# Performance work log

Hardware: AMD Instinct MI355X
Metric: run time of the kernel (lower is better)

Reference implementation:

```python
import jax, jax.numpy as jnp
import numpy as np
import math

HIDDEN = 2048
NUM_HEADS = 16
HEAD_SIZE = HIDDEN // NUM_HEADS
BATCH = 2
SEQ = 2048


def setup_inputs() -> dict:
    key = jax.random.key(0)
    k_x, k_wq, k_bq, k_wo, k_bo = jax.random.split(key, 5)
    scale_in = 1.0 / math.sqrt(HIDDEN)
    return {
        "x": jax.random.normal(k_x, (BATCH, SEQ, HIDDEN), dtype=jnp.float32),
        # torch Linear stored as W[out,in]; we keep the jax-friendly transpose [in,out]
        "Wqkv": jax.random.normal(k_wq, (HIDDEN, 3 * HIDDEN), dtype=jnp.float32) * scale_in,
        "bqkv": jax.random.normal(k_bq, (3 * HIDDEN,), dtype=jnp.float32) * 0.01,
        "Wo": jax.random.normal(k_wo, (HIDDEN, HIDDEN), dtype=jnp.float32) * scale_in,
        "bo": jax.random.normal(k_bo, (HIDDEN,), dtype=jnp.float32) * 0.01,
    }


def reference(x, Wqkv, bqkv, Wo, bo):
    b, s, _ = x.shape
    # fused QKV projection; channel layout is (three, num_heads, head_size)
    kqv = x @ Wqkv + bqkv                      # [b, s, 3*hidden]
    kqv = kqv.reshape(b, s, 3, NUM_HEADS, HEAD_SIZE)
    q = kqv[:, :, 0]                           # [b, s, n, h]
    k = kqv[:, :, 1]
    v = kqv[:, :, 2]
    # scores[b, n, s_key, t_query] = K_s . Q_t, scaled
    scores = jnp.einsum('bsnh,btnh->bnst', k, q) / math.sqrt(HEAD_SIZE)
    # faithful to original: keep upper triangle (key <= query), masked entries are exactly -10000
    ones = jnp.ones_like(scores)
    scores = jnp.triu(scores) + (-10000.0) * jnp.tril(ones, k=-1)
    attn = jax.nn.softmax(scores, axis=2)      # softmax over key dim
    out = jnp.einsum('bnkq,bknh->bqnh', attn, v)  # [b, s, n, h]
    out = out.reshape(b, s, NUM_HEADS * HEAD_SIZE)
    return out @ Wo + bo
```

## Files before the change

kernel.cpp:

```cpp
#include <hip/hip_runtime.h>
#include <hip/hip_bf16.h>

typedef __hip_bfloat16 bf16;
typedef __attribute__((ext_vector_type(8))) short short8;
typedef __attribute__((ext_vector_type(8))) unsigned short ushort8;
typedef __attribute__((ext_vector_type(4))) float floatx4;

#define BATCH 2
#define S_LEN 2048
#define NHEAD 16
#define HD 128
#define HIDDEN 2048
#define QSCALE 0.12754435f

static __device__ __forceinline__ unsigned short f2bf(float f) {
    union { float f; unsigned int u; } c; c.f = f;
    unsigned int u = c.u;
    unsigned int rounded = u + 0x7FFF + ((u >> 16) & 1);
    return (unsigned short)(rounded >> 16);
}

__global__ __launch_bounds__(256) void cast_f32_bf16(const float* __restrict__ src,
                                                     bf16* __restrict__ dst) {
    int i = (blockIdx.x * 256 + threadIdx.x) * 8;
    float4 a = *(const float4*)&src[i];
    float4 b = *(const float4*)&src[i + 4];
    ushort8 o;
    o[0] = f2bf(a.x); o[1] = f2bf(a.y); o[2] = f2bf(a.z); o[3] = f2bf(a.w);
    o[4] = f2bf(b.x); o[5] = f2bf(b.y); o[6] = f2bf(b.z); o[7] = f2bf(b.w);
    *(ushort8*)&dst[i] = o;
}

__global__ __launch_bounds__(256) void cast_transpose(const float* __restrict__ src,
                                                      bf16* __restrict__ dst,
                                                      int R, int C) {
    __shared__ unsigned short t[32][33];
    int tx = threadIdx.x & 31, ty = threadIdx.x >> 5;
    int c0 = blockIdx.x * 32, r0 = blockIdx.y * 32;
#pragma unroll
    for (int i = 0; i < 4; i++) {
        int r = r0 + ty + i * 8;
        t[ty + i * 8][tx] = f2bf(src[(size_t)r * C + c0 + tx]);
    }
    __syncthreads();
#pragma unroll
    for (int i = 0; i < 4; i++) {
        int cc = c0 + ty + i * 8;
        ((unsigned short*)dst)[(size_t)cc * R + r0 + tx] = t[tx][ty + i * 8];
    }
}

__global__ __launch_bounds__(256) void gemm_bt(const bf16* __restrict__ A,
                                               const bf16* __restrict__ Bt,
                                               const float* __restrict__ bias,
                                               float* __restrict__ C,
                                               bf16* __restrict__ Qb,
                                               bf16* __restrict__ Kb,
                                               bf16* __restrict__ Vt,
                                               int M, int N, int K, int mode) {
    __shared__ __align__(16) bf16 As[128 * 32];
    __shared__ __align__(16) bf16 Bs[128 * 32];

    int tid = threadIdx.x;
    int wave = tid >> 6, lane = tid & 63;
    int quad = lane >> 4, lr = lane & 15;
    int wm = wave >> 1, wn = wave & 1;
    int m0 = blockIdx.y * 128, n0 = blockIdx.x * 128;

    const floatx4 fzero = {0.f, 0.f, 0.f, 0.f};
    floatx4 acc[4][4];
#pragma unroll
    for (int i = 0; i < 4; i++)
#pragma unroll
        for (int j = 0; j < 4; j++) acc[i][j] = fzero;

    int rsub = lane >> 2;
    int csub = (lane & 3) * 8;
    const bf16* gA0 = A + (size_t)(m0 + wave * 32 + rsub) * K + csub;
    const bf16* gA1 = gA0 + (size_t)16 * K;
    const bf16* gB0 = Bt + (size_t)(n0 + wave * 32 + rsub) * K + csub;
    const bf16* gB1 = gB0 + (size_t)16 * K;
    bf16* lA0 = As + wave * 1024;
    bf16* lA1 = As + wave * 1024 + 512;
    bf16* lB0 = Bs + wave * 1024;
    bf16* lB1 = Bs + wave * 1024 + 512;

    for (int kt = 0; kt < K; kt += 32) {
        __builtin_amdgcn_global_load_lds(
            (const __attribute__((address_space(1))) void*)(gA0 + kt),
            (__attribute__((address_space(3))) void*)lA0, 16, 0, 0);
        __builtin_amdgcn_global_load_lds(
            (const __attribute__((address_space(1))) void*)(gA1 + kt),
            (__attribute__((address_space(3))) void*)lA1, 16, 0, 0);
        __builtin_amdgcn_global_load_lds(
            (const __attribute__((address_space(1))) void*)(gB0 + kt),
            (__attribute__((address_space(3))) void*)lB0, 16, 0, 0);
        __builtin_amdgcn_global_load_lds(
            (const __attribute__((address_space(1))) void*)(gB1 + kt),
            (__attribute__((address_space(3))) void*)lB1, 16, 0, 0);
        __syncthreads();

        short8 aF[4], bF[4];
#pragma unroll
        for (int i = 0; i < 4; i++)
            aF[i] = *(const short8*)(As + (wm * 64 + i * 16 + lr) * 32 + quad * 8);
#pragma unroll
        for (int j = 0; j < 4; j++)
            bF[j] = *(const short8*)(Bs + (wn * 64 + j * 16 + lr) * 32 + quad * 8);
#pragma unroll
        for (int i = 0; i < 4; i++)
#pragma unroll
            for (int j = 0; j < 4; j++)
                acc[i][j] = __builtin_amdgcn_mfma_f32_16x16x32_bf16(aF[i], bF[j], acc[i][j], 0, 0, 0);
        __syncthreads();
    }

#pragma unroll
    for (int i = 0; i < 4; i++) {
#pragma unroll
        for (int j = 0; j < 4; j++) {
            int gcn = n0 + wn * 64 + j * 16 + lr;
            float bv = bias[gcn];
#pragma unroll
            for (int reg = 0; reg < 4; reg++) {
                int gm = m0 + wm * 64 + i * 16 + quad * 4 + reg;
                float v = acc[i][j][reg] + bv;
                if (mode == 0) {
                    int t = gcn >> 11, hh = (gcn >> 7) & 15, d = gcn & 127;
                    int bb = gm >> 11, s = gm & 2047;
                    size_t hb = (size_t)(bb * NHEAD + hh);
                    if (t == 0) {
                        Qb[(hb * S_LEN + s) * HD + d] = __float2bfloat16(v * QSCALE);
                    } else if (t == 1) {
                        Kb[(hb * S_LEN + s) * HD + d] = __float2bfloat16(v);
                    } else {
                        Vt[(hb * HD + d) * S_LEN + s] = __float2bfloat16(v);
                    }
                } else {
                    C[(size_t)gm * N + gcn] = v;
                }
            }
        }
    }
}

__global__ __launch_bounds__(256, 1) void attn_kernel(const bf16* __restrict__ Qb,
                                                      const bf16* __restrict__ Kb,
                                                      const bf16* __restrict__ Vt,
                                                      bf16* __restrict__ Obuf) {
    __shared__ __align__(16) bf16 Ks[128][136];
    __shared__ __align__(16) bf16 Vs[128][136];
    __shared__ __align__(16) bf16 Ps[4][32][144];

    int tid = threadIdx.x;
    int wave = tid >> 6, lane = tid & 63;
    int quad = lane >> 4, lr = lane & 15;
    int p = blockIdx.x, head = blockIdx.y, b = blockIdx.z;
    size_t hb = (size_t)(b * NHEAD + head);
    const bf16* Qbase = Qb + hb * S_LEN * HD;
    const bf16* Kbase = Kb + hb * S_LEN * HD;
    const bf16* Vbase = Vt + hb * (size_t)HD * S_LEN;

    const floatx4 fzero = {0.f, 0.f, 0.f, 0.f};
    const float MASKV = -30000.f;

    int pr = 0, pc = 0;
    ushort8 kpre[8], vpre[8];

    for (int sub = 0; sub < 2; sub++) {
        int qt = sub ? (15 - p) : p;
        int q0 = qt * 128;
        int niter = qt + 1;

        short8 qF[2][4];
#pragma unroll
        for (int mt = 0; mt < 2; mt++)
#pragma unroll
            for (int kc = 0; kc < 4; kc++)
                qF[mt][kc] = *(const short8*)&Qbase[(size_t)(q0 + wave * 32 + mt * 16 + lr) * HD + kc * 32 + quad * 8];

        floatx4 Oacc[2][8];
        float mrow[2][4], lrow[2][4];
#pragma unroll
        for (int mt = 0; mt < 2; mt++) {
#pragma unroll
            for (int dn = 0; dn < 8; dn++) Oacc[mt][dn] = fzero;
#pragma unroll
            for (int r = 0; r < 4; r++) { mrow[mt][r] = -30000.f; lrow[mt][r] = 0.f; }
        }

#pragma unroll
        for (int i = 0; i < 8; i++) {
            int idx = tid + i * 256;
            pr = idx >> 4; pc = (idx & 15) * 8;
            kpre[i] = *(const ushort8*)&Kbase[(size_t)pr * HD + pc];
            vpre[i] = *(const ushort8*)&Vbase[(size_t)pr * S_LEN + pc];
        }

        for (int kt = 0; kt < niter; kt++) {
            int ks0 = kt * 128;
            __syncthreads();
#pragma unroll
            for (int i = 0; i < 8; i++) {
                int idx = tid + i * 256;
                pr = idx >> 4; pc = (idx & 15) * 8;
                *(ushort8*)&Ks[pr][pc] = kpre[i];
                *(ushort8*)&Vs[pr][pc] = vpre[i];
            }
            __syncthreads();
            if (kt + 1 < niter) {
                int ns0 = ks0 + 128;
#pragma unroll
                for (int i = 0; i < 8; i++) {
                    int idx = tid + i * 256;
                    pr = idx >> 4; pc = (idx & 15) * 8;
                    kpre[i] = *(const ushort8*)&Kbase[(size_t)(ns0 + pr) * HD + pc];
                    vpre[i] = *(const ushort8*)&Vbase[(size_t)pr * S_LEN + ns0 + pc];
                }
            }

            floatx4 sc[2][8];
#pragma unroll
            for (int mt = 0; mt < 2; mt++)
#pragma unroll
                for (int nt = 0; nt < 8; nt++) sc[mt][nt] = fzero;
#pragma unroll
            for (int kc = 0; kc < 4; kc++)
#pragma unroll
                for (int nt = 0; nt < 8; nt++) {
                    short8 kf = *(const short8*)&Ks[nt * 16 + lr][kc * 32 + quad * 8];
#pragma unroll
                    for (int mt = 0; mt < 2; mt++)
                        sc[mt][nt] = __builtin_amdgcn_mfma_f32_16x16x32_bf16(qF[mt][kc], kf, sc[mt][nt], 0, 0, 0);
                }
            if (kt == qt) {
#pragma unroll
                for (int mt = 0; mt < 2; mt++)
#pragma unroll
                    for (int nt = 0; nt < 8; nt++)
#pragma unroll
                        for (int reg = 0; reg < 4; reg++) {
                            int qg = wave * 32 + mt * 16 + quad * 4 + reg;
                            int kg = nt * 16 + lr;
                            if (kg > qg) sc[mt][nt][reg] = MASKV;
                        }
            }
#pragma unroll
            for (int mt = 0; mt < 2; mt++) {
                float pm[4], alpha[4], rs[4];
#pragma unroll
                for (int r = 0; r < 4; r++) {
                    pm[r] = sc[mt][0][r];
#pragma unroll
                    for (int nt = 1; nt < 8; nt++) pm[r] = fmaxf(pm[r], sc[mt][nt][r]);
                }
#pragma unroll
                for (int off = 1; off < 16; off <<= 1)
#pragma unroll
                    for (int r = 0; r < 4; r++) pm[r] = fmaxf(pm[r], __shfl_xor(pm[r], off, 64));
#pragma unroll
                for (int r = 0; r < 4; r++) {
                    float mn = fmaxf(mrow[mt][r], pm[r]);
                    alpha[r] = __builtin_amdgcn_exp2f(mrow[mt][r] - mn);
                    mrow[mt][r] = mn;
                    rs[r] = 0.f;
                }
#pragma unroll
                for (int nt = 0; nt < 8; nt++)
#pragma unroll
                    for (int r = 0; r < 4; r++) {
                        float pv = __builtin_amdgcn_exp2f(sc[mt][nt][r] - mrow[mt][r]);
                        rs[r] += pv;
                        Ps[wave][mt * 16 + quad * 4 + r][nt * 16 + lr] = __float2bfloat16(pv);
                    }
#pragma unroll
                for (int off = 1; off < 16; off <<= 1)
#pragma unroll
                    for (int r = 0; r < 4; r++) rs[r] += __shfl_xor(rs[r], off, 64);
#pragma unroll
                for (int r = 0; r < 4; r++) lrow[mt][r] = lrow[mt][r] * alpha[r] + rs[r];
#pragma unroll
                for (int dn = 0; dn < 8; dn++)
#pragma unroll
                    for (int r = 0; r < 4; r++) Oacc[mt][dn][r] *= alpha[r];
            }
#pragma unroll
            for (int st = 0; st < 4; st++) {
                short8 aP[2];
#pragma unroll
                for (int mt = 0; mt < 2; mt++)
                    aP[mt] = *(const short8*)&Ps[wave][mt * 16 + lr][st * 32 + quad * 8];
#pragma unroll
                for (int dn = 0; dn < 8; dn++) {
                    short8 vf = *(const short8*)&Vs[dn * 16 + lr][st * 32 + quad * 8];
#pragma unroll
                    for (int mt = 0; mt < 2; mt++)
                        Oacc[mt][dn] = __builtin_amdgcn_mfma_f32_16x16x32_bf16(aP[mt], vf, Oacc[mt][dn], 0, 0, 0);
                }
            }
        }

#pragma unroll
        for (int mt = 0; mt < 2; mt++)
#pragma unroll
            for (int reg = 0; reg < 4; reg++) {
                float inv = 1.0f / lrow[mt][reg];
                int qg = q0 + wave * 32 + mt * 16 + quad * 4 + reg;
#pragma unroll
                for (int dn = 0; dn < 8; dn++) {
                    int d = dn * 16 + lr;
                    Obuf[((size_t)(b * S_LEN + qg)) * HIDDEN + head * HD + d] =
                        __float2bfloat16(Oacc[mt][dn][reg] * inv);
                }
            }
    }
}

extern "C" void kernel_launch(void* const* d_in, const int* in_sizes, int n_in,
                              void* d_out, int out_size, void* d_ws, size_t ws_size,
                              hipStream_t stream) {
    (void)in_sizes; (void)n_in; (void)out_size; (void)ws_size;
    const float* x    = (const float*)d_in[0];
    const float* Wqkv = (const float*)d_in[1];
    const float* bqkv = (const float*)d_in[2];
    const float* Wo   = (const float*)d_in[3];
    const float* bo   = (const float*)d_in[4];
    float* out = (float*)d_out;

    bf16* ws = (bf16*)d_ws;
    bf16* Xb    = ws;
    bf16* Obuf  = ws;
    bf16* WqkvT = ws + (size_t)8388608;
    bf16* WoT   = WqkvT;
    bf16* Qb    = WqkvT + (size_t)12582912;
    bf16* Kb    = Qb + (size_t)8388608;
    bf16* Vt    = Kb + (size_t)8388608;

    cast_f32_bf16<<<4096, 256, 0, stream>>>(x, Xb);
    cast_transpose<<<dim3(192, 64), 256, 0, stream>>>(Wqkv, WqkvT, 2048, 6144);
    gemm_bt<<<dim3(48, 32), 256, 0, stream>>>(Xb, WqkvT, bqkv, nullptr,
                                              Qb, Kb, Vt, 4096, 6144, 2048, 0);
    cast_transpose<<<dim3(64, 64), 256, 0, stream>>>(Wo, WoT, 2048, 2048);
    attn_kernel<<<dim3(8, 16, 2), 256, 0, stream>>>(Qb, Kb, Vt, Obuf);
    gemm_bt<<<dim3(16, 32), 256, 0, stream>>>(Obuf, WoT, bo, out,
                                              nullptr, nullptr, nullptr, 4096, 2048, 2048, 1);
}
```

Before: 458.1 us.

## Load K/V tiles directly into LDS with XOR-swizzled layout

```diff
diff --git a/kernel.cpp b/kernel.cpp
--- a/kernel.cpp
+++ b/kernel.cpp
@@ -144,17 +144,19 @@
     }
 }
 
+#define PSTR 134
 __global__ __launch_bounds__(256, 1) void attn_kernel(const bf16* __restrict__ Qb,
                                                       const bf16* __restrict__ Kb,
                                                       const bf16* __restrict__ Vt,
                                                       bf16* __restrict__ Obuf) {
-    __shared__ __align__(16) bf16 Ks[128][136];
-    __shared__ __align__(16) bf16 Vs[128][136];
-    __shared__ __align__(16) bf16 Ps[4][32][144];
+    __shared__ __align__(16) bf16 Ks[128 * 128];
+    __shared__ __align__(16) bf16 Vs[128 * 128];
+    __shared__ __align__(16) bf16 Ps[4][32 * PSTR];
 
     int tid = threadIdx.x;
     int wave = tid >> 6, lane = tid & 63;
     int quad = lane >> 4, lr = lane & 15;
+    int srow = lane >> 4;
     int p = blockIdx.x, head = blockIdx.y, b = blockIdx.z;
     size_t hb = (size_t)(b * NHEAD + head);
     const bf16* Qbase = Qb + hb * S_LEN * HD;
@@ -164,9 +166,6 @@
     const floatx4 fzero = {0.f, 0.f, 0.f, 0.f};
     const float MASKV = -30000.f;
 
-    int pr = 0, pc = 0;
-    ushort8 kpre[8], vpre[8];
-
     for (int sub = 0; sub < 2; sub++) {
         int qt = sub ? (15 - p) : p;
         int q0 = qt * 128;
@@ -189,35 +188,21 @@
             for (int r = 0; r < 4; r++) { mrow[mt][r] = -30000.f; lrow[mt][r] = 0.f; }
         }
 
-#pragma unroll
-        for (int i = 0; i < 8; i++) {
-            int idx = tid + i * 256;
-            pr = idx >> 4; pc = (idx & 15) * 8;
-            kpre[i] = *(const ushort8*)&Kbase[(size_t)pr * HD + pc];
-            vpre[i] = *(const ushort8*)&Vbase[(size_t)pr * S_LEN + pc];
-        }
-
         for (int kt = 0; kt < niter; kt++) {
             int ks0 = kt * 128;
             __syncthreads();
 #pragma unroll
             for (int i = 0; i < 8; i++) {
-                int idx = tid + i * 256;
-                pr = idx >> 4; pc = (idx & 15) * 8;
-                *(ushort8*)&Ks[pr][pc] = kpre[i];
-                *(ushort8*)&Vs[pr][pc] = vpre[i];
+                int rl = wave * 32 + i * 4 + srow;
+                int gc = lr ^ (rl & 15);
+                __builtin_amdgcn_global_load_lds(
+                    (const __attribute__((address_space(1))) void*)(Kbase + (size_t)(ks0 + rl) * HD + gc * 8),
+                    (__attribute__((address_space(3))) void*)(Ks + (wave * 32 + i * 4) * 128), 16, 0, 0);
+                __builtin_amdgcn_global_load_lds(
+                    (const __attribute__((address_space(1))) void*)(Vbase + (size_t)rl * S_LEN + ks0 + gc * 8),
+                    (__attribute__((address_space(3))) void*)(Vs + (wave * 32 + i * 4) * 128), 16, 0, 0);
             }
             __syncthreads();
-            if (kt + 1 < niter) {
-                int ns0 = ks0 + 128;
-#pragma unroll
-                for (int i = 0; i < 8; i++) {
-                    int idx = tid + i * 256;
-                    pr = idx >> 4; pc = (idx & 15) * 8;
-                    kpre[i] = *(const ushort8*)&Kbase[(size_t)(ns0 + pr) * HD + pc];
-                    vpre[i] = *(const ushort8*)&Vbase[(size_t)pr * S_LEN + ns0 + pc];
-                }
-            }
 
             floatx4 sc[2][8];
 #pragma unroll
@@ -228,7 +213,7 @@
             for (int kc = 0; kc < 4; kc++)
 #pragma unroll
                 for (int nt = 0; nt < 8; nt++) {
-                    short8 kf = *(const short8*)&Ks[nt * 16 + lr][kc * 32 + quad * 8];
+                    short8 kf = *(const short8*)&Ks[(nt * 16 + lr) * 128 + (((kc * 4 + quad) ^ lr) & 15) * 8];
 #pragma unroll
                     for (int mt = 0; mt < 2; mt++)
                         sc[mt][nt] = __builtin_amdgcn_mfma_f32_16x16x32_bf16(qF[mt][kc], kf, sc[mt][nt], 0, 0, 0);
@@ -271,7 +256,7 @@
                     for (int r = 0; r < 4; r++) {
                         float pv = __builtin_amdgcn_exp2f(sc[mt][nt][r] - mrow[mt][r]);
                         rs[r] += pv;
-                        Ps[wave][mt * 16 + quad * 4 + r][nt * 16 + lr] = __float2bfloat16(pv);
+                        Ps[wave][(mt * 16 + quad * 4 + r) * PSTR + nt * 16 + lr] = __float2bfloat16(pv);
                     }
 #pragma unroll
                 for (int off = 1; off < 16; off <<= 1)
@@ -289,10 +274,10 @@
                 short8 aP[2];
 #pragma unroll
                 for (int mt = 0; mt < 2; mt++)
-                    aP[mt] = *(const short8*)&Ps[wave][mt * 16 + lr][st * 32 + quad * 8];
+                    aP[mt] = *(const short8*)&Ps[wave][(mt * 16 + lr) * PSTR + st * 32 + quad * 8];
 #pragma unroll
                 for (int dn = 0; dn < 8; dn++) {
-                    short8 vf = *(const short8*)&Vs[dn * 16 + lr][st * 32 + quad * 8];
+                    short8 vf = *(const short8*)&Vs[(dn * 16 + lr) * 128 + (((st * 4 + quad) ^ lr) & 15) * 8];
 #pragma unroll
                     for (int mt = 0; mt < 2; mt++)
                         Oacc[mt][dn] = __builtin_amdgcn_mfma_f32_16x16x32_bf16(aP[mt], vf, Oacc[mt][dn], 0, 0, 0);
```

Result: no change. 462.8 us (+1.0%).
